# Performance work log

Measured on AMD Instinct MI355X. Metric: run time of the kernel, lower is better.

## Reference

```python
import jax, jax.numpy as jnp
import numpy as np

NUM_EXPERTS = 64
TOP_K = 2
B, S, EMB, MLP = 4, 2048, 1024, 2048


def setup_inputs() -> dict:
    key = jax.random.key(0)
    k1, k2, k3, k4, k5 = jax.random.split(key, 5)
    inputs = jax.random.normal(k1, (B, S, EMB), dtype=jnp.float32)
    gate_kernel = jax.random.normal(k2, (EMB, NUM_EXPERTS), dtype=jnp.float32) / np.sqrt(EMB)
    w0 = jax.random.normal(k3, (NUM_EXPERTS, EMB, MLP), dtype=jnp.float32) / np.sqrt(EMB)
    w1 = jax.random.normal(k4, (NUM_EXPERTS, EMB, MLP), dtype=jnp.float32) / np.sqrt(EMB)
    wo = jax.random.normal(k5, (NUM_EXPERTS, MLP, EMB), dtype=jnp.float32) / np.sqrt(MLP)
    return {"inputs": inputs, "gate_kernel": gate_kernel, "w0": w0, "w1": w1, "wo": wo}


def reference(inputs, gate_kernel, w0, w1, wo):
    b, s, e = inputs.shape
    x = inputs.reshape(b * s, e)                                  # [T, E]
    # Router (DenseGeneral gate)
    gate_logits = jnp.einsum('te,ex->tx', x, gate_kernel)         # [T, X]
    # permute(): top-k gating + sort tokens by expert
    weights, selected = jax.lax.top_k(gate_logits, TOP_K)         # [T, K]
    weights = jax.nn.softmax(weights.astype(jnp.float32), axis=-1)
    flat_experts = selected.reshape(-1)                           # [T*K]
    sort_idx = jnp.argsort(flat_experts)                          # [T*K]
    token_idx = sort_idx // TOP_K
    sorted_x = jnp.take(x, token_idx, axis=0)                     # [T*K, E]
    group_sizes = jnp.bincount(flat_experts, length=NUM_EXPERTS).astype(jnp.int32)
    # grouped GEMMs (gated FFN: silu(x@w0) * (x@w1) @ wo)
    h0 = jax.lax.ragged_dot(sorted_x, w0, group_sizes)            # [T*K, M]
    h1 = jax.lax.ragged_dot(sorted_x, w1, group_sizes)            # [T*K, M]
    inter = jax.nn.silu(h0) * h1
    out_sorted = jax.lax.ragged_dot(inter, wo, group_sizes)       # [T*K, E]
    # unpermute(): restore token order, weighted combine over top-k
    unsorted = jnp.take(out_sorted, jnp.argsort(sort_idx), axis=0)
    per_tok = unsorted.reshape(b * s, TOP_K, e)
    out = jnp.einsum('BKE,BK->BE', per_tok.astype(jnp.float32), weights)
    return out.reshape(b, s, e)
```

## Files before the change

kernel.cpp:

```cpp
#include <hip/hip_runtime.h>
#include <hip/hip_bf16.h>
#include <math.h>

#define NTOK   8192
#define NEXP   64
#define EMBD   1024
#define MLPD   2048
#define TOPK   2
#define NFLAT  (NTOK * TOPK)
#define BKD    32
#define MAXCH  8

typedef __attribute__((ext_vector_type(4)))  float  f32x4;
typedef __attribute__((ext_vector_type(16))) float  f32x16;
typedef __attribute__((ext_vector_type(8)))  __bf16 bf16x8;

__device__ __forceinline__ void gl16(const void* g, void* lds_base) {
  __builtin_amdgcn_global_load_lds(
      (const __attribute__((address_space(1))) unsigned int*)g,
      (__attribute__((address_space(3))) unsigned int*)lds_base, 16, 0, 0);
}
__device__ __forceinline__ void lgkm0_bar() {
  asm volatile("s_waitcnt lgkmcnt(0)" ::: "memory");
  __builtin_amdgcn_sched_barrier(0);
  __builtin_amdgcn_s_barrier();
}

#define OFF_COUNTS 0
#define OFF_BASE   256
#define OFF_RUN    512
#define OFF_EFLAT  1024
#define OFF_WFLAT  (1024 + 65536)
#define OFF_ROWTOK (1024 + 2 * 65536)
#define OFF_F2R    (1024 + 3 * 65536)
#define OFF_INTER  (1024 + 4 * 65536)
#define OFF_OS     (OFF_INTER + (size_t)NFLAT * MLPD * 2)
#define NEED_F32   (OFF_OS + (size_t)NFLAT * EMBD * 4)

__global__ __launch_bounds__(256) void router_topk(
    const float* __restrict__ x, const float* __restrict__ gk,
    int* __restrict__ e_flat, float* __restrict__ w_flat) {
  int t = blockIdx.x * 4 + (threadIdx.x >> 6);
  int l = threadIdx.x & 63;
  const float* xr = x + (size_t)t * EMBD;
  float acc = 0.f;
  #pragma unroll 8
  for (int i = 0; i < EMBD; ++i)
    acc = fmaf(xr[i], gk[i * NEXP + l], acc);
  float m = acc;
  for (int o = 32; o; o >>= 1) m = fmaxf(m, __shfl_xor(m, o));
  unsigned long long b1 = __ballot(acc == m);
  int i1 = __ffsll(b1) - 1;
  float v2 = (l == i1) ? -INFINITY : acc;
  float m2 = v2;
  for (int o = 32; o; o >>= 1) m2 = fmaxf(m2, __shfl_xor(m2, o));
  unsigned long long b2 = __ballot(v2 == m2);
  int i2 = __ffsll(b2) - 1;
  if (l == 0) {
    float e2 = expf(m2 - m);
    float inv = 1.f / (1.f + e2);
    e_flat[2 * t] = i1;  e_flat[2 * t + 1] = i2;
    w_flat[2 * t] = inv; w_flat[2 * t + 1] = e2 * inv;
  }
}

__global__ void hist_k(const int* __restrict__ ef, int* __restrict__ counts) {
  int j = blockIdx.x * 256 + threadIdx.x;
  if (j < NFLAT) atomicAdd(&counts[ef[j]], 1);
}

__global__ void scan_k(const int* __restrict__ counts, int* __restrict__ base) {
  if (threadIdx.x == 0) {
    int s = 0;
    for (int e = 0; e < NEXP; ++e) { base[e] = s; s += counts[e]; }
  }
}

__global__ void scatter_k(const int* __restrict__ ef, const int* __restrict__ base,
                          int* __restrict__ run, int* __restrict__ rowtok,
                          int* __restrict__ f2r) {
  int j = blockIdx.x * 256 + threadIdx.x;
  if (j < NFLAT) {
    int e = ef[j];
    int r = base[e] + atomicAdd(&run[e], 1);
    f2r[j] = r;
    rowtok[r] = j >> 1;
  }
}

__global__ __launch_bounds__(256, 3) void gemm1_k(
    const float* __restrict__ x, const float* __restrict__ w0,
    const float* __restrict__ w1, const int* __restrict__ counts,
    const int* __restrict__ base, const int* __restrict__ rowtok,
    __hip_bfloat16* __restrict__ inter) {
  int e = blockIdx.z;
  int Me = counts[e];
  int mc = blockIdx.y;
  if (mc * 128 >= Me) return;
  int rs = base[e];
  int nb = blockIdx.x * 64;
  int t = threadIdx.x;
  int wv = t >> 6, l = t & 63;
  int wr = wv >> 1, wc = wv & 1;
  int lo = l & 31, hi = l >> 5;

  __shared__ float Ash[4096];
  __shared__ float Bsh[2][4096];

  const float* abase0 = x;
  const float* abase1 = x;
  const float* wbase  = w0;
  if (wv < 2) {
    int g0 = wv * 2, g1 = wv * 2 + 1;
    int r0 = mc * 128 + g0 * 32 + lo; r0 = r0 < Me ? r0 : Me - 1;
    int r1 = mc * 128 + g1 * 32 + lo; r1 = r1 < Me ? r1 : Me - 1;
    abase0 = x + (size_t)rowtok[rs + r0] * EMBD + hi * 4;
    abase1 = x + (size_t)rowtok[rs + r1] * EMBD + hi * 4;
  } else {
    const float* w = (wv == 3) ? w1 : w0;
    wbase = w + (size_t)e * EMBD * MLPD + nb + (l & 15) * 4 + (size_t)(l >> 4) * MLPD;
  }
  int matofs = (wv & 1) * 2048;

  auto STAGE_A = [&](int kk) {
    #pragma unroll
    for (int h = 0; h < 4; ++h) {
      gl16(abase0 + kk + h * 8, &Ash[((wv * 2 + 0) * 4 + h) * 256]);
      gl16(abase1 + kk + h * 8, &Ash[((wv * 2 + 1) * 4 + h) * 256]);
    }
  };
  auto STAGE_B = [&](int buf, int kk) {
    #pragma unroll
    for (int j = 0; j < 8; ++j)
      gl16(wbase + (size_t)(kk + j * 4) * MLPD, &Bsh[buf][matofs + j * 256]);
  };

  f32x16 acc0[2], acc1[2];
  #pragma unroll
  for (int g = 0; g < 2; ++g)
    #pragma unroll
    for (int r = 0; r < 16; ++r) { acc0[g][r] = 0.f; acc1[g][r] = 0.f; }

  if (wv < 2) STAGE_A(0);
  else { STAGE_B(0, 0); STAGE_B(1, BKD); }

  const int NT = EMBD / BKD;
  for (int ks = 0; ks < NT; ++ks) {
    if (wv >= 2 && ks + 1 < NT) asm volatile("s_waitcnt vmcnt(8)" ::: "memory");
    else                        asm volatile("s_waitcnt vmcnt(0)" ::: "memory");
    __builtin_amdgcn_s_barrier();

    f32x4 a[2][2][2];
    #pragma unroll
    for (int g = 0; g < 2; ++g)
      #pragma unroll
      for (int kh = 0; kh < 2; ++kh) {
        int idx = (((wr * 2 + g) * 4 + kh * 2 + hi) * 256) + lo * 4;
        a[g][kh][0] = *(const f32x4*)&Ash[idx];
        a[g][kh][1] = *(const f32x4*)&Ash[idx + 128];
      }
    float b[2][2][8];
    const float* bb = Bsh[ks & 1];
    #pragma unroll
    for (int m = 0; m < 2; ++m)
      #pragma unroll
      for (int kh = 0; kh < 2; ++kh) {
        int bi = m * 2048 + (kh * 16 + hi * 8) * 64 + wc * 32 + lo;
        #pragma unroll
        for (int q = 0; q < 8; ++q) b[m][kh][q] = bb[bi + q * 64];
      }
    lgkm0_bar();
    if (wv < 2) { if (ks + 1 < NT) STAGE_A((ks + 1) * BKD); }
    else if (ks + 2 < NT) STAGE_B(ks & 1, (ks + 2) * BKD);

    bf16x8 av[2][2], bv[2][2];
    #pragma unroll
    for (int g = 0; g < 2; ++g)
      #pragma unroll
      for (int kh = 0; kh < 2; ++kh)
        #pragma unroll
        for (int q = 0; q < 4; ++q) {
          av[g][kh][q]     = (__bf16)a[g][kh][0][q];
          av[g][kh][4 + q] = (__bf16)a[g][kh][1][q];
        }
    #pragma unroll
    for (int m = 0; m < 2; ++m)
      #pragma unroll
      for (int kh = 0; kh < 2; ++kh)
        #pragma unroll
        for (int q = 0; q < 8; ++q) bv[m][kh][q] = (__bf16)b[m][kh][q];
    #pragma unroll
    for (int kh = 0; kh < 2; ++kh)
      #pragma unroll
      for (int g = 0; g < 2; ++g) {
        acc0[g] = __builtin_amdgcn_mfma_f32_32x32x16_bf16(av[g][kh], bv[0][kh], acc0[g], 0, 0, 0);
        acc1[g] = __builtin_amdgcn_mfma_f32_32x32x16_bf16(av[g][kh], bv[1][kh], acc1[g], 0, 0, 0);
      }
  }

  #pragma unroll
  for (int g = 0; g < 2; ++g)
    #pragma unroll
    for (int r = 0; r < 16; ++r) {
      int rl = mc * 128 + wr * 64 + g * 32 + (r & 3) + 8 * (r >> 2) + 4 * hi;
      if (rl < Me) {
        float h0 = acc0[g][r], h1 = acc1[g][r];
        float s = h0 / (1.f + expf(-h0)) * h1;
        inter[(size_t)(rs + rl) * MLPD + nb + wc * 32 + lo] = (__hip_bfloat16)s;
      }
    }
}

template <typename OS_T>
__global__ __launch_bounds__(256, 4) void gemm2_k(
    const __hip_bfloat16* __restrict__ inter, const float* __restrict__ wo,
    const int* __restrict__ counts, const int* __restrict__ base,
    OS_T* __restrict__ os) {
  int e = blockIdx.z;
  int Me = counts[e];
  int mc = blockIdx.y;
  if (mc * 128 >= Me) return;
  int rs = base[e];
  int nb = blockIdx.x * 64;
  int t = threadIdx.x;
  int wv = t >> 6, l = t & 63;
  int wr = wv >> 1, wc = wv & 1;
  int lo = l & 31, hi = l >> 5;

  __shared__ __bf16 A2[2][4096];
  __shared__ float  B2[2][2048];

  const __hip_bfloat16* ab0 = inter;
  const __hip_bfloat16* ab1 = inter;
  const float* wbase = wo;
  if (wv < 2) {
    int g0 = wv * 2, g1 = wv * 2 + 1;
    int r0 = mc * 128 + g0 * 32 + lo; r0 = r0 < Me ? r0 : Me - 1;
    int r1 = mc * 128 + g1 * 32 + lo; r1 = r1 < Me ? r1 : Me - 1;
    ab0 = inter + (size_t)(rs + r0) * MLPD + hi * 8;
    ab1 = inter + (size_t)(rs + r1) * MLPD + hi * 8;
  } else {
    wbase = wo + (size_t)e * MLPD * EMBD + nb + (l & 15) * 4 + (size_t)(l >> 4) * EMBD;
  }
  int jofs = (wv & 1) * 4;

  auto STAGE = [&](int buf, int kk) {
    if (wv < 2) {
      #pragma unroll
      for (int kh = 0; kh < 2; ++kh) {
        gl16(ab0 + kk + kh * 16, &A2[buf][((wv * 2 + 0) * 2 + kh) * 512]);
        gl16(ab1 + kk + kh * 16, &A2[buf][((wv * 2 + 1) * 2 + kh) * 512]);
      }
    } else {
      #pragma unroll
      for (int j = 0; j < 4; ++j)
        gl16(wbase + (size_t)(kk + (jofs + j) * 4) * EMBD, &B2[buf][(jofs + j) * 256]);
    }
  };

  f32x16 acc[2];
  #pragma unroll
  for (int g = 0; g < 2; ++g)
    #pragma unroll
    for (int r = 0; r < 16; ++r) acc[g][r] = 0.f;

  STAGE(0, 0);
  STAGE(1, BKD);
  const int NT = MLPD / BKD;
  for (int ks = 0; ks < NT; ++ks) {
    if (ks + 1 < NT) asm volatile("s_waitcnt vmcnt(4)" ::: "memory");
    else             asm volatile("s_waitcnt vmcnt(0)" ::: "memory");
    __builtin_amdgcn_s_barrier();

    bf16x8 av[2][2];
    #pragma unroll
    for (int g = 0; g < 2; ++g)
      #pragma unroll
      for (int kh = 0; kh < 2; ++kh)
        av[g][kh] = *(const bf16x8*)&A2[ks & 1][(((wr * 2 + g) * 2 + kh) * 512) + l * 8];
    float b[2][8];
    #pragma unroll
    for (int kh = 0; kh < 2; ++kh) {
      int bi = (kh * 16 + hi * 8) * 64 + wc * 32 + lo;
      #pragma unroll
      for (int q = 0; q < 8; ++q) b[kh][q] = B2[ks & 1][bi + q * 64];
    }
    lgkm0_bar();
    if (ks + 2 < NT) STAGE(ks & 1, (ks + 2) * BKD);

    bf16x8 bv[2];
    #pragma unroll
    for (int kh = 0; kh < 2; ++kh)
      #pragma unroll
      for (int q = 0; q < 8; ++q) bv[kh][q] = (__bf16)b[kh][q];
    #pragma unroll
    for (int kh = 0; kh < 2; ++kh)
      #pragma unroll
      for (int g = 0; g < 2; ++g)
        acc[g] = __builtin_amdgcn_mfma_f32_32x32x16_bf16(av[g][kh], bv[kh], acc[g], 0, 0, 0);
  }

  #pragma unroll
  for (int g = 0; g < 2; ++g)
    #pragma unroll
    for (int r = 0; r < 16; ++r) {
      int rl = mc * 128 + wr * 64 + g * 32 + (r & 3) + 8 * (r >> 2) + 4 * hi;
      if (rl < Me)
        os[(size_t)(rs + rl) * EMBD + nb + wc * 32 + lo] = (OS_T)acc[g][r];
    }
}

template <typename OS_T>
__global__ __launch_bounds__(256) void combine_k(
    const OS_T* __restrict__ os, const int* __restrict__ f2r,
    const float* __restrict__ wf, float* __restrict__ out) {
  int t = blockIdx.x;
  int c = threadIdx.x * 4;
  int r0 = f2r[2 * t], r1 = f2r[2 * t + 1];
  float wa = wf[2 * t], wb = wf[2 * t + 1];
  const OS_T* pa = os + (size_t)r0 * EMBD + c;
  const OS_T* pb = os + (size_t)r1 * EMBD + c;
  float4 o;
  o.x = wa * (float)pa[0] + wb * (float)pb[0];
  o.y = wa * (float)pa[1] + wb * (float)pb[1];
  o.z = wa * (float)pa[2] + wb * (float)pb[2];
  o.w = wa * (float)pa[3] + wb * (float)pb[3];
  *(float4*)(out + (size_t)t * EMBD + c) = o;
}

extern "C" void kernel_launch(void* const* d_in, const int* in_sizes, int n_in,
                              void* d_out, int out_size, void* d_ws, size_t ws_size,
                              hipStream_t stream) {
  const float* x  = (const float*)d_in[0];
  const float* gk = (const float*)d_in[1];
  const float* w0 = (const float*)d_in[2];
  const float* w1 = (const float*)d_in[3];
  const float* wo = (const float*)d_in[4];
  float* out = (float*)d_out;
  char* ws = (char*)d_ws;

  int*   counts = (int*)(ws + OFF_COUNTS);
  int*   basep  = (int*)(ws + OFF_BASE);
  int*   run    = (int*)(ws + OFF_RUN);
  int*   ef     = (int*)(ws + OFF_EFLAT);
  float* wfl    = (float*)(ws + OFF_WFLAT);
  int*   rowtok = (int*)(ws + OFF_ROWTOK);
  int*   f2r    = (int*)(ws + OFF_F2R);
  __hip_bfloat16* inter = (__hip_bfloat16*)(ws + OFF_INTER);

  hipMemsetAsync(ws, 0, 1024, stream);
  router_topk<<<NTOK / 4, 256, 0, stream>>>(x, gk, ef, wfl);
  hist_k<<<NFLAT / 256, 256, 0, stream>>>(ef, counts);
  scan_k<<<1, 64, 0, stream>>>(counts, basep);
  scatter_k<<<NFLAT / 256, 256, 0, stream>>>(ef, basep, run, rowtok, f2r);
  gemm1_k<<<dim3(MLPD / 64, MAXCH, NEXP), 256, 0, stream>>>(x, w0, w1, counts, basep, rowtok, inter);

  if (ws_size >= NEED_F32) {
    float* os = (float*)(ws + OFF_OS);
    gemm2_k<float><<<dim3(EMBD / 64, MAXCH, NEXP), 256, 0, stream>>>(inter, wo, counts, basep, os);
    combine_k<float><<<NTOK, 256, 0, stream>>>(os, f2r, wfl, out);
  } else {
    __hip_bfloat16* os = (__hip_bfloat16*)(ws + OFF_OS);
    gemm2_k<__hip_bfloat16><<<dim3(EMBD / 64, MAXCH, NEXP), 256, 0, stream>>>(inter, wo, counts, basep, os);
    combine_k<__hip_bfloat16><<<NTOK, 256, 0, stream>>>(os, f2r, wfl, out);
  }
}
```

Measured before the change: 1.087 ms.

## Load weight tiles straight into registers and double-buffer activations in LDS

Both grouped GEMM kernels change how they stage data. The weight (B) operand now goes straight from global memory into registers, prefetched two K-steps ahead, instead of being staged through LDS by dedicated waves. All four waves now share loading the activation (A) tile into a double-buffered LDS array. This removes the LDS round trip and the second barrier per step for B, at the cost of more registers (hence the lower occupancy hints in launch bounds) and duplicate B loads across the two row-waves.

```diff
diff --git a/kernel.cpp b/kernel.cpp
--- a/kernel.cpp
+++ b/kernel.cpp
@@ -19,11 +19,6 @@
   __builtin_amdgcn_global_load_lds(
       (const __attribute__((address_space(1))) unsigned int*)g,
       (__attribute__((address_space(3))) unsigned int*)lds_base, 16, 0, 0);
-}
-__device__ __forceinline__ void lgkm0_bar() {
-  asm volatile("s_waitcnt lgkmcnt(0)" ::: "memory");
-  __builtin_amdgcn_sched_barrier(0);
-  __builtin_amdgcn_s_barrier();
 }
 
 #define OFF_COUNTS 0
@@ -88,7 +83,7 @@
   }
 }
 
-__global__ __launch_bounds__(256, 3) void gemm1_k(
+__global__ __launch_bounds__(256, 2) void gemm1_k(
     const float* __restrict__ x, const float* __restrict__ w0,
     const float* __restrict__ w1, const int* __restrict__ counts,
     const int* __restrict__ base, const int* __restrict__ rowtok,
@@ -103,100 +98,88 @@
   int wv = t >> 6, l = t & 63;
   int wr = wv >> 1, wc = wv & 1;
   int lo = l & 31, hi = l >> 5;
-
-  __shared__ float Ash[4096];
-  __shared__ float Bsh[2][4096];
-
-  const float* abase0 = x;
-  const float* abase1 = x;
-  const float* wbase  = w0;
-  if (wv < 2) {
-    int g0 = wv * 2, g1 = wv * 2 + 1;
-    int r0 = mc * 128 + g0 * 32 + lo; r0 = r0 < Me ? r0 : Me - 1;
-    int r1 = mc * 128 + g1 * 32 + lo; r1 = r1 < Me ? r1 : Me - 1;
-    abase0 = x + (size_t)rowtok[rs + r0] * EMBD + hi * 4;
-    abase1 = x + (size_t)rowtok[rs + r1] * EMBD + hi * 4;
-  } else {
-    const float* w = (wv == 3) ? w1 : w0;
-    wbase = w + (size_t)e * EMBD * MLPD + nb + (l & 15) * 4 + (size_t)(l >> 4) * MLPD;
-  }
-  int matofs = (wv & 1) * 2048;
-
-  auto STAGE_A = [&](int kk) {
-    #pragma unroll
-    for (int h = 0; h < 4; ++h) {
-      gl16(abase0 + kk + h * 8, &Ash[((wv * 2 + 0) * 4 + h) * 256]);
-      gl16(abase1 + kk + h * 8, &Ash[((wv * 2 + 1) * 4 + h) * 256]);
-    }
-  };
-  auto STAGE_B = [&](int buf, int kk) {
-    #pragma unroll
-    for (int j = 0; j < 8; ++j)
-      gl16(wbase + (size_t)(kk + j * 4) * MLPD, &Bsh[buf][matofs + j * 256]);
-  };
-
+  int hi8 = hi * 8;
+
+  __shared__ float Ash[2][4096];
+
+  int rga = mc * 128 + wv * 32 + lo; rga = rga < Me ? rga : Me - 1;
+  const float* abase = x + (size_t)rowtok[rs + rga] * EMBD + hi * 4;
+  const float* bsrc0 = w0 + (size_t)e * EMBD * MLPD + nb + wc * 32 + lo;
+  const float* bsrc1 = w1 + (size_t)e * EMBD * MLPD + nb + wc * 32 + lo;
+
+  float br[2][2][2][8];
   f32x16 acc0[2], acc1[2];
   #pragma unroll
   for (int g = 0; g < 2; ++g)
     #pragma unroll
     for (int r = 0; r < 16; ++r) { acc0[g][r] = 0.f; acc1[g][r] = 0.f; }
 
-  if (wv < 2) STAGE_A(0);
-  else { STAGE_B(0, 0); STAGE_B(1, BKD); }
-
   const int NT = EMBD / BKD;
-  for (int ks = 0; ks < NT; ++ks) {
-    if (wv >= 2 && ks + 1 < NT) asm volatile("s_waitcnt vmcnt(8)" ::: "memory");
-    else                        asm volatile("s_waitcnt vmcnt(0)" ::: "memory");
-    __builtin_amdgcn_s_barrier();
-
-    f32x4 a[2][2][2];
-    #pragma unroll
-    for (int g = 0; g < 2; ++g)
-      #pragma unroll
-      for (int kh = 0; kh < 2; ++kh) {
-        int idx = (((wr * 2 + g) * 4 + kh * 2 + hi) * 256) + lo * 4;
-        a[g][kh][0] = *(const f32x4*)&Ash[idx];
-        a[g][kh][1] = *(const f32x4*)&Ash[idx + 128];
-      }
-    float b[2][2][8];
-    const float* bb = Bsh[ks & 1];
-    #pragma unroll
-    for (int m = 0; m < 2; ++m)
-      #pragma unroll
-      for (int kh = 0; kh < 2; ++kh) {
-        int bi = m * 2048 + (kh * 16 + hi * 8) * 64 + wc * 32 + lo;
-        #pragma unroll
-        for (int q = 0; q < 8; ++q) b[m][kh][q] = bb[bi + q * 64];
-      }
-    lgkm0_bar();
-    if (wv < 2) { if (ks + 1 < NT) STAGE_A((ks + 1) * BKD); }
-    else if (ks + 2 < NT) STAGE_B(ks & 1, (ks + 2) * BKD);
-
-    bf16x8 av[2][2], bv[2][2];
-    #pragma unroll
-    for (int g = 0; g < 2; ++g)
-      #pragma unroll
-      for (int kh = 0; kh < 2; ++kh)
-        #pragma unroll
-        for (int q = 0; q < 4; ++q) {
-          av[g][kh][q]     = (__bf16)a[g][kh][0][q];
-          av[g][kh][4 + q] = (__bf16)a[g][kh][1][q];
-        }
-    #pragma unroll
-    for (int m = 0; m < 2; ++m)
-      #pragma unroll
-      for (int kh = 0; kh < 2; ++kh)
-        #pragma unroll
-        for (int q = 0; q < 8; ++q) bv[m][kh][q] = (__bf16)b[m][kh][q];
+
+  #pragma unroll
+  for (int h = 0; h < 4; ++h)
+    gl16(abase + h * 8, &Ash[0][(wv * 4 + h) * 256]);
+  #pragma unroll
+  for (int m = 0; m < 2; ++m)
     #pragma unroll
     for (int kh = 0; kh < 2; ++kh)
       #pragma unroll
-      for (int g = 0; g < 2; ++g) {
-        acc0[g] = __builtin_amdgcn_mfma_f32_32x32x16_bf16(av[g][kh], bv[0][kh], acc0[g], 0, 0, 0);
-        acc1[g] = __builtin_amdgcn_mfma_f32_32x32x16_bf16(av[g][kh], bv[1][kh], acc1[g], 0, 0, 0);
+      for (int q = 0; q < 8; ++q) {
+        br[0][m][kh][q] = (m ? bsrc1 : bsrc0)[(size_t)(kh * 16 + hi8 + q) * MLPD];
+        br[1][m][kh][q] = (m ? bsrc1 : bsrc0)[(size_t)(BKD + kh * 16 + hi8 + q) * MLPD];
       }
-  }
+
+#define G1_PHASE(cur, ks)                                                           \
+  {                                                                                 \
+    if ((ks) + 1 < NT) asm volatile("s_waitcnt vmcnt(32)" ::: "memory");            \
+    else               asm volatile("s_waitcnt vmcnt(0)" ::: "memory");             \
+    __builtin_amdgcn_s_barrier();                                                   \
+    bf16x8 bv0[2], bv1[2];                                                          \
+    _Pragma("unroll")                                                               \
+    for (int kh = 0; kh < 2; ++kh)                                                  \
+      _Pragma("unroll")                                                             \
+      for (int q = 0; q < 8; ++q) {                                                 \
+        bv0[kh][q] = (__bf16)br[cur][0][kh][q];                                     \
+        bv1[kh][q] = (__bf16)br[cur][1][kh][q];                                     \
+      }                                                                             \
+    __builtin_amdgcn_sched_barrier(0);                                              \
+    if ((ks) + 1 < NT) {                                                            \
+      _Pragma("unroll")                                                             \
+      for (int h = 0; h < 4; ++h)                                                   \
+        gl16(abase + ((ks) + 1) * BKD + h * 8, &Ash[(cur) ^ 1][(wv * 4 + h) * 256]);\
+    }                                                                               \
+    __builtin_amdgcn_sched_barrier(0);                                              \
+    if ((ks) + 2 < NT) {                                                            \
+      _Pragma("unroll")                                                             \
+      for (int m = 0; m < 2; ++m)                                                   \
+        _Pragma("unroll")                                                           \
+        for (int kh = 0; kh < 2; ++kh)                                              \
+          _Pragma("unroll")                                                         \
+          for (int q = 0; q < 8; ++q)                                               \
+            br[cur][m][kh][q] = (m ? bsrc1 : bsrc0)[                                \
+                (size_t)(((ks) + 2) * BKD + kh * 16 + hi8 + q) * MLPD];             \
+    }                                                                               \
+    __builtin_amdgcn_sched_barrier(0);                                              \
+    _Pragma("unroll")                                                               \
+    for (int g = 0; g < 2; ++g)                                                     \
+      _Pragma("unroll")                                                             \
+      for (int kh = 0; kh < 2; ++kh) {                                              \
+        int idx = ((wr * 2 + g) * 4 + kh * 2 + hi) * 256 + lo * 4;                  \
+        f32x4 q0 = *(const f32x4*)&Ash[cur][idx];                                   \
+        f32x4 q1 = *(const f32x4*)&Ash[cur][idx + 128];                             \
+        bf16x8 av;                                                                  \
+        _Pragma("unroll")                                                           \
+        for (int q = 0; q < 4; ++q) { av[q] = (__bf16)q0[q]; av[4 + q] = (__bf16)q1[q]; } \
+        acc0[g] = __builtin_amdgcn_mfma_f32_32x32x16_bf16(av, bv0[kh], acc0[g], 0, 0, 0); \
+        acc1[g] = __builtin_amdgcn_mfma_f32_32x32x16_bf16(av, bv1[kh], acc1[g], 0, 0, 0); \
+      }                                                                             \
+  }
+
+  for (int ks = 0; ks < NT; ks += 2) {
+    G1_PHASE(0, ks);
+    G1_PHASE(1, ks + 1);
+  }
+#undef G1_PHASE
 
   #pragma unroll
   for (int g = 0; g < 2; ++g)
@@ -212,7 +195,7 @@
 }
 
 template <typename OS_T>
-__global__ __launch_bounds__(256, 4) void gemm2_k(
+__global__ __launch_bounds__(256, 3) void gemm2_k(
     const __hip_bfloat16* __restrict__ inter, const float* __restrict__ wo,
     const int* __restrict__ counts, const int* __restrict__ base,
     OS_T* __restrict__ os) {
@@ -226,79 +209,73 @@
   int wv = t >> 6, l = t & 63;
   int wr = wv >> 1, wc = wv & 1;
   int lo = l & 31, hi = l >> 5;
+  int hi8 = hi * 8;
 
   __shared__ __bf16 A2[2][4096];
-  __shared__ float  B2[2][2048];
-
-  const __hip_bfloat16* ab0 = inter;
-  const __hip_bfloat16* ab1 = inter;
-  const float* wbase = wo;
-  if (wv < 2) {
-    int g0 = wv * 2, g1 = wv * 2 + 1;
-    int r0 = mc * 128 + g0 * 32 + lo; r0 = r0 < Me ? r0 : Me - 1;
-    int r1 = mc * 128 + g1 * 32 + lo; r1 = r1 < Me ? r1 : Me - 1;
-    ab0 = inter + (size_t)(rs + r0) * MLPD + hi * 8;
-    ab1 = inter + (size_t)(rs + r1) * MLPD + hi * 8;
-  } else {
-    wbase = wo + (size_t)e * MLPD * EMBD + nb + (l & 15) * 4 + (size_t)(l >> 4) * EMBD;
-  }
-  int jofs = (wv & 1) * 4;
-
-  auto STAGE = [&](int buf, int kk) {
-    if (wv < 2) {
-      #pragma unroll
-      for (int kh = 0; kh < 2; ++kh) {
-        gl16(ab0 + kk + kh * 16, &A2[buf][((wv * 2 + 0) * 2 + kh) * 512]);
-        gl16(ab1 + kk + kh * 16, &A2[buf][((wv * 2 + 1) * 2 + kh) * 512]);
-      }
-    } else {
-      #pragma unroll
-      for (int j = 0; j < 4; ++j)
-        gl16(wbase + (size_t)(kk + (jofs + j) * 4) * EMBD, &B2[buf][(jofs + j) * 256]);
+
+  int rga = mc * 128 + wv * 32 + lo; rga = rga < Me ? rga : Me - 1;
+  const __hip_bfloat16* ab = inter + (size_t)(rs + rga) * MLPD + hi8;
+  const float* bsrc = wo + (size_t)e * MLPD * EMBD + nb + wc * 32 + lo;
+
+  float br[2][2][8];
+  f32x16 acc[2];
+  #pragma unroll
+  for (int g = 0; g < 2; ++g)
+    #pragma unroll
+    for (int r = 0; r < 16; ++r) acc[g][r] = 0.f;
+
+  const int NT = MLPD / BKD;
+
+  #pragma unroll
+  for (int kh = 0; kh < 2; ++kh)
+    gl16(ab + kh * 16, &A2[0][(wv * 2 + kh) * 512]);
+  #pragma unroll
+  for (int kh = 0; kh < 2; ++kh)
+    #pragma unroll
+    for (int q = 0; q < 8; ++q) {
+      br[0][kh][q] = bsrc[(size_t)(kh * 16 + hi8 + q) * EMBD];
+      br[1][kh][q] = bsrc[(size_t)(BKD + kh * 16 + hi8 + q) * EMBD];
     }
-  };
-
-  f32x16 acc[2];
-  #pragma unroll
-  for (int g = 0; g < 2; ++g)
-    #pragma unroll
-    for (int r = 0; r < 16; ++r) acc[g][r] = 0.f;
-
-  STAGE(0, 0);
-  STAGE(1, BKD);
-  const int NT = MLPD / BKD;
-  for (int ks = 0; ks < NT; ++ks) {
-    if (ks + 1 < NT) asm volatile("s_waitcnt vmcnt(4)" ::: "memory");
-    else             asm volatile("s_waitcnt vmcnt(0)" ::: "memory");
-    __builtin_amdgcn_s_barrier();
-
-    bf16x8 av[2][2];
-    #pragma unroll
-    for (int g = 0; g < 2; ++g)
-      #pragma unroll
-      for (int kh = 0; kh < 2; ++kh)
-        av[g][kh] = *(const bf16x8*)&A2[ks & 1][(((wr * 2 + g) * 2 + kh) * 512) + l * 8];
-    float b[2][8];
-    #pragma unroll
-    for (int kh = 0; kh < 2; ++kh) {
-      int bi = (kh * 16 + hi * 8) * 64 + wc * 32 + lo;
-      #pragma unroll
-      for (int q = 0; q < 8; ++q) b[kh][q] = B2[ks & 1][bi + q * 64];
-    }
-    lgkm0_bar();
-    if (ks + 2 < NT) STAGE(ks & 1, (ks + 2) * BKD);
-
-    bf16x8 bv[2];
-    #pragma unroll
-    for (int kh = 0; kh < 2; ++kh)
-      #pragma unroll
-      for (int q = 0; q < 8; ++q) bv[kh][q] = (__bf16)b[kh][q];
-    #pragma unroll
-    for (int kh = 0; kh < 2; ++kh)
-      #pragma unroll
-      for (int g = 0; g < 2; ++g)
-        acc[g] = __builtin_amdgcn_mfma_f32_32x32x16_bf16(av[g][kh], bv[kh], acc[g], 0, 0, 0);
-  }
+
+#define G2_PHASE(cur, ks)                                                           \
+  {                                                                                 \
+    if ((ks) + 1 < NT) asm volatile("s_waitcnt vmcnt(16)" ::: "memory");            \
+    else               asm volatile("s_waitcnt vmcnt(0)" ::: "memory");             \
+    __builtin_amdgcn_s_barrier();                                                   \
+    bf16x8 bv[2];                                                                   \
+    _Pragma("unroll")                                                               \
+    for (int kh = 0; kh < 2; ++kh)                                                  \
+      _Pragma("unroll")                                                             \
+      for (int q = 0; q < 8; ++q) bv[kh][q] = (__bf16)br[cur][kh][q];               \
+    __builtin_amdgcn_sched_barrier(0);                                              \
+    if ((ks) + 1 < NT) {                                                            \
+      _Pragma("unroll")                                                             \
+      for (int kh = 0; kh < 2; ++kh)                                                \
+        gl16(ab + ((ks) + 1) * BKD + kh * 16, &A2[(cur) ^ 1][(wv * 2 + kh) * 512]); \
+    }                                                                               \
+    __builtin_amdgcn_sched_barrier(0);                                              \
+    if ((ks) + 2 < NT) {                                                            \
+      _Pragma("unroll")                                                             \
+      for (int kh = 0; kh < 2; ++kh)                                                \
+        _Pragma("unroll")                                                           \
+        for (int q = 0; q < 8; ++q)                                                 \
+          br[cur][kh][q] = bsrc[(size_t)(((ks) + 2) * BKD + kh * 16 + hi8 + q) * EMBD]; \
+    }                                                                               \
+    __builtin_amdgcn_sched_barrier(0);                                              \
+    _Pragma("unroll")                                                               \
+    for (int g = 0; g < 2; ++g)                                                     \
+      _Pragma("unroll")                                                             \
+      for (int kh = 0; kh < 2; ++kh) {                                              \
+        bf16x8 av = *(const bf16x8*)&A2[cur][((wr * 2 + g) * 2 + kh) * 512 + l * 8];\
+        acc[g] = __builtin_amdgcn_mfma_f32_32x32x16_bf16(av, bv[kh], acc[g], 0, 0, 0); \
+      }                                                                             \
+  }
+
+  for (int ks = 0; ks < NT; ks += 2) {
+    G2_PHASE(0, ks);
+    G2_PHASE(1, ks + 1);
+  }
+#undef G2_PHASE
 
   #pragma unroll
   for (int g = 0; g < 2; ++g)
```

Result: slower. 1.140 ms (+4.9%).

## Pre-convert activations to bf16 and triple-buffer both grouped GEMM pipelines

Applied to the files above, without the earlier changes.

A new kernel converts the input activations to bf16 once, so gemm1 gathers half as many bytes per row and no longer converts A in its inner loop. Both GEMMs move from double to triple-buffered LDS staging, with all four waves sharing the A and B loads. The next-next tile is issued right after the barrier, which removes the second LDS-drain barrier per iteration. The cost is an extra conversion pass over x, more LDS per block, and lower occupancy hints. The bf16 buffer reuses the output scratch region, which is safe only because gemm1 finishes before gemm2 writes there.

```diff
diff --git a/kernel.cpp b/kernel.cpp
--- a/kernel.cpp
+++ b/kernel.cpp
@@ -19,11 +19,6 @@
   __builtin_amdgcn_global_load_lds(
       (const __attribute__((address_space(1))) unsigned int*)g,
       (__attribute__((address_space(3))) unsigned int*)lds_base, 16, 0, 0);
-}
-__device__ __forceinline__ void lgkm0_bar() {
-  asm volatile("s_waitcnt lgkmcnt(0)" ::: "memory");
-  __builtin_amdgcn_sched_barrier(0);
-  __builtin_amdgcn_s_barrier();
 }
 
 #define OFF_COUNTS 0
@@ -35,7 +30,19 @@
 #define OFF_F2R    (1024 + 3 * 65536)
 #define OFF_INTER  (1024 + 4 * 65536)
 #define OFF_OS     (OFF_INTER + (size_t)NFLAT * MLPD * 2)
+#define OFF_XB     OFF_OS
 #define NEED_F32   (OFF_OS + (size_t)NFLAT * EMBD * 4)
+
+__global__ __launch_bounds__(256) void cvt_x_k(const float* __restrict__ x,
+                                               __bf16* __restrict__ xb) {
+  size_t i = ((size_t)blockIdx.x * 256 + threadIdx.x) * 8;
+  f32x4 f0 = *(const f32x4*)(x + i);
+  f32x4 f1 = *(const f32x4*)(x + i + 4);
+  bf16x8 v;
+  #pragma unroll
+  for (int q = 0; q < 4; ++q) { v[q] = (__bf16)f0[q]; v[4 + q] = (__bf16)f1[q]; }
+  *(bf16x8*)(xb + i) = v;
+}
 
 __global__ __launch_bounds__(256) void router_topk(
     const float* __restrict__ x, const float* __restrict__ gk,
@@ -88,8 +95,8 @@
   }
 }
 
-__global__ __launch_bounds__(256, 3) void gemm1_k(
-    const float* __restrict__ x, const float* __restrict__ w0,
+__global__ __launch_bounds__(256, 2) void gemm1_k(
+    const __bf16* __restrict__ xb, const float* __restrict__ w0,
     const float* __restrict__ w1, const int* __restrict__ counts,
     const int* __restrict__ base, const int* __restrict__ rowtok,
     __hip_bfloat16* __restrict__ inter) {
@@ -104,36 +111,26 @@
   int wr = wv >> 1, wc = wv & 1;
   int lo = l & 31, hi = l >> 5;
 
-  __shared__ float Ash[4096];
-  __shared__ float Bsh[2][4096];
-
-  const float* abase0 = x;
-  const float* abase1 = x;
-  const float* wbase  = w0;
-  if (wv < 2) {
-    int g0 = wv * 2, g1 = wv * 2 + 1;
-    int r0 = mc * 128 + g0 * 32 + lo; r0 = r0 < Me ? r0 : Me - 1;
-    int r1 = mc * 128 + g1 * 32 + lo; r1 = r1 < Me ? r1 : Me - 1;
-    abase0 = x + (size_t)rowtok[rs + r0] * EMBD + hi * 4;
-    abase1 = x + (size_t)rowtok[rs + r1] * EMBD + hi * 4;
-  } else {
-    const float* w = (wv == 3) ? w1 : w0;
-    wbase = w + (size_t)e * EMBD * MLPD + nb + (l & 15) * 4 + (size_t)(l >> 4) * MLPD;
-  }
-  int matofs = (wv & 1) * 2048;
-
-  auto STAGE_A = [&](int kk) {
-    #pragma unroll
-    for (int h = 0; h < 4; ++h) {
-      gl16(abase0 + kk + h * 8, &Ash[((wv * 2 + 0) * 4 + h) * 256]);
-      gl16(abase1 + kk + h * 8, &Ash[((wv * 2 + 1) * 4 + h) * 256]);
-    }
+  __shared__ __bf16 A1[3][4096];
+  __shared__ float  B1[3][4096];
+
+  int rga = mc * 128 + wv * 32 + lo; rga = rga < Me ? rga : Me - 1;
+  const __bf16* abase = xb + (size_t)rowtok[rs + rga] * EMBD + hi * 8;
+  int bm = wv >> 1, bk0 = (wv & 1) * 16;
+  const float* wsel = bm ? w1 : w0;
+  const float* wbase = wsel + (size_t)e * EMBD * MLPD + nb + (l & 15) * 4 +
+                       (size_t)(l >> 4) * MLPD;
+
+  auto STAGE = [&](int ks, int buf) {
+    int kk = ks * BKD;
+    #pragma unroll
+    for (int kh = 0; kh < 2; ++kh)
+      gl16(abase + kk + kh * 16, &A1[buf][(wv * 2 + kh) * 512]);
+    #pragma unroll
+    for (int j = 0; j < 4; ++j)
+      gl16(wbase + (size_t)(kk + bk0 + j * 4) * MLPD,
+           &B1[buf][bm * 2048 + (bk0 + j * 4) * 64]);
   };
-  auto STAGE_B = [&](int buf, int kk) {
-    #pragma unroll
-    for (int j = 0; j < 8; ++j)
-      gl16(wbase + (size_t)(kk + j * 4) * MLPD, &Bsh[buf][matofs + j * 256]);
-  };
 
   f32x16 acc0[2], acc1[2];
   #pragma unroll
@@ -141,61 +138,49 @@
     #pragma unroll
     for (int r = 0; r < 16; ++r) { acc0[g][r] = 0.f; acc1[g][r] = 0.f; }
 
-  if (wv < 2) STAGE_A(0);
-  else { STAGE_B(0, 0); STAGE_B(1, BKD); }
-
   const int NT = EMBD / BKD;
+  STAGE(0, 0);
+  STAGE(1, 1);
+  int bufR = 0, bufW = 2;
   for (int ks = 0; ks < NT; ++ks) {
-    if (wv >= 2 && ks + 1 < NT) asm volatile("s_waitcnt vmcnt(8)" ::: "memory");
-    else                        asm volatile("s_waitcnt vmcnt(0)" ::: "memory");
+    if (ks + 1 < NT) asm volatile("s_waitcnt vmcnt(6)" ::: "memory");
+    else             asm volatile("s_waitcnt vmcnt(0)" ::: "memory");
+    __builtin_amdgcn_sched_barrier(0);
     __builtin_amdgcn_s_barrier();
-
-    f32x4 a[2][2][2];
+    if (ks + 2 < NT) STAGE(ks + 2, bufW);
+
+    bf16x8 av[2][2];
     #pragma unroll
     for (int g = 0; g < 2; ++g)
       #pragma unroll
-      for (int kh = 0; kh < 2; ++kh) {
-        int idx = (((wr * 2 + g) * 4 + kh * 2 + hi) * 256) + lo * 4;
-        a[g][kh][0] = *(const f32x4*)&Ash[idx];
-        a[g][kh][1] = *(const f32x4*)&Ash[idx + 128];
-      }
+      for (int kh = 0; kh < 2; ++kh)
+        av[g][kh] = *(const bf16x8*)&A1[bufR][((wr * 2 + g) * 2 + kh) * 512 + l * 8];
     float b[2][2][8];
-    const float* bb = Bsh[ks & 1];
     #pragma unroll
     for (int m = 0; m < 2; ++m)
       #pragma unroll
       for (int kh = 0; kh < 2; ++kh) {
         int bi = m * 2048 + (kh * 16 + hi * 8) * 64 + wc * 32 + lo;
         #pragma unroll
-        for (int q = 0; q < 8; ++q) b[m][kh][q] = bb[bi + q * 64];
+        for (int q = 0; q < 8; ++q) b[m][kh][q] = B1[bufR][bi + q * 64];
       }
-    lgkm0_bar();
-    if (wv < 2) { if (ks + 1 < NT) STAGE_A((ks + 1) * BKD); }
-    else if (ks + 2 < NT) STAGE_B(ks & 1, (ks + 2) * BKD);
-
-    bf16x8 av[2][2], bv[2][2];
-    #pragma unroll
-    for (int g = 0; g < 2; ++g)
-      #pragma unroll
-      for (int kh = 0; kh < 2; ++kh)
-        #pragma unroll
-        for (int q = 0; q < 4; ++q) {
-          av[g][kh][q]     = (__bf16)a[g][kh][0][q];
-          av[g][kh][4 + q] = (__bf16)a[g][kh][1][q];
-        }
-    #pragma unroll
-    for (int m = 0; m < 2; ++m)
-      #pragma unroll
-      for (int kh = 0; kh < 2; ++kh)
-        #pragma unroll
-        for (int q = 0; q < 8; ++q) bv[m][kh][q] = (__bf16)b[m][kh][q];
+    bf16x8 bv0[2], bv1[2];
+    #pragma unroll
+    for (int kh = 0; kh < 2; ++kh)
+      #pragma unroll
+      for (int q = 0; q < 8; ++q) {
+        bv0[kh][q] = (__bf16)b[0][kh][q];
+        bv1[kh][q] = (__bf16)b[1][kh][q];
+      }
     #pragma unroll
     for (int kh = 0; kh < 2; ++kh)
       #pragma unroll
       for (int g = 0; g < 2; ++g) {
-        acc0[g] = __builtin_amdgcn_mfma_f32_32x32x16_bf16(av[g][kh], bv[0][kh], acc0[g], 0, 0, 0);
-        acc1[g] = __builtin_amdgcn_mfma_f32_32x32x16_bf16(av[g][kh], bv[1][kh], acc1[g], 0, 0, 0);
+        acc0[g] = __builtin_amdgcn_mfma_f32_32x32x16_bf16(av[g][kh], bv0[kh], acc0[g], 0, 0, 0);
+        acc1[g] = __builtin_amdgcn_mfma_f32_32x32x16_bf16(av[g][kh], bv1[kh], acc1[g], 0, 0, 0);
       }
+    bufR = bufR == 2 ? 0 : bufR + 1;
+    bufW = bufW == 2 ? 0 : bufW + 1;
   }
 
   #pragma unroll
@@ -212,7 +197,7 @@
 }
 
 template <typename OS_T>
-__global__ __launch_bounds__(256, 4) void gemm2_k(
+__global__ __launch_bounds__(256, 3) void gemm2_k(
     const __hip_bfloat16* __restrict__ inter, const float* __restrict__ wo,
     const int* __restrict__ counts, const int* __restrict__ base,
     OS_T* __restrict__ os) {
@@ -227,35 +212,23 @@
   int wr = wv >> 1, wc = wv & 1;
   int lo = l & 31, hi = l >> 5;
 
-  __shared__ __bf16 A2[2][4096];
-  __shared__ float  B2[2][2048];
-
-  const __hip_bfloat16* ab0 = inter;
-  const __hip_bfloat16* ab1 = inter;
-  const float* wbase = wo;
-  if (wv < 2) {
-    int g0 = wv * 2, g1 = wv * 2 + 1;
-    int r0 = mc * 128 + g0 * 32 + lo; r0 = r0 < Me ? r0 : Me - 1;
-    int r1 = mc * 128 + g1 * 32 + lo; r1 = r1 < Me ? r1 : Me - 1;
-    ab0 = inter + (size_t)(rs + r0) * MLPD + hi * 8;
-    ab1 = inter + (size_t)(rs + r1) * MLPD + hi * 8;
-  } else {
-    wbase = wo + (size_t)e * MLPD * EMBD + nb + (l & 15) * 4 + (size_t)(l >> 4) * EMBD;
-  }
-  int jofs = (wv & 1) * 4;
-
-  auto STAGE = [&](int buf, int kk) {
-    if (wv < 2) {
-      #pragma unroll
-      for (int kh = 0; kh < 2; ++kh) {
-        gl16(ab0 + kk + kh * 16, &A2[buf][((wv * 2 + 0) * 2 + kh) * 512]);
-        gl16(ab1 + kk + kh * 16, &A2[buf][((wv * 2 + 1) * 2 + kh) * 512]);
-      }
-    } else {
-      #pragma unroll
-      for (int j = 0; j < 4; ++j)
-        gl16(wbase + (size_t)(kk + (jofs + j) * 4) * EMBD, &B2[buf][(jofs + j) * 256]);
-    }
+  __shared__ __bf16 A2[3][4096];
+  __shared__ float  B2[3][2048];
+
+  int rga = mc * 128 + wv * 32 + lo; rga = rga < Me ? rga : Me - 1;
+  const __bf16* abase = (const __bf16*)inter + (size_t)(rs + rga) * MLPD + hi * 8;
+  const float* wbase = wo + (size_t)e * MLPD * EMBD + nb + (l & 15) * 4 +
+                       (size_t)(l >> 4) * EMBD;
+
+  auto STAGE = [&](int ks, int buf) {
+    int kk = ks * BKD;
+    #pragma unroll
+    for (int kh = 0; kh < 2; ++kh)
+      gl16(abase + kk + kh * 16, &A2[buf][(wv * 2 + kh) * 512]);
+    #pragma unroll
+    for (int j = 0; j < 2; ++j)
+      gl16(wbase + (size_t)(kk + wv * 8 + j * 4) * EMBD,
+           &B2[buf][(wv * 8 + j * 4) * 64]);
   };
 
   f32x16 acc[2];
@@ -264,30 +237,30 @@
     #pragma unroll
     for (int r = 0; r < 16; ++r) acc[g][r] = 0.f;
 
+  const int NT = MLPD / BKD;
   STAGE(0, 0);
-  STAGE(1, BKD);
-  const int NT = MLPD / BKD;
+  STAGE(1, 1);
+  int bufR = 0, bufW = 2;
   for (int ks = 0; ks < NT; ++ks) {
     if (ks + 1 < NT) asm volatile("s_waitcnt vmcnt(4)" ::: "memory");
     else             asm volatile("s_waitcnt vmcnt(0)" ::: "memory");
+    __builtin_amdgcn_sched_barrier(0);
     __builtin_amdgcn_s_barrier();
+    if (ks + 2 < NT) STAGE(ks + 2, bufW);
 
     bf16x8 av[2][2];
     #pragma unroll
     for (int g = 0; g < 2; ++g)
       #pragma unroll
       for (int kh = 0; kh < 2; ++kh)
-        av[g][kh] = *(const bf16x8*)&A2[ks & 1][(((wr * 2 + g) * 2 + kh) * 512) + l * 8];
+        av[g][kh] = *(const bf16x8*)&A2[bufR][((wr * 2 + g) * 2 + kh) * 512 + l * 8];
     float b[2][8];
     #pragma unroll
     for (int kh = 0; kh < 2; ++kh) {
       int bi = (kh * 16 + hi * 8) * 64 + wc * 32 + lo;
       #pragma unroll
-      for (int q = 0; q < 8; ++q) b[kh][q] = B2[ks & 1][bi + q * 64];
+      for (int q = 0; q < 8; ++q) b[kh][q] = B2[bufR][bi + q * 64];
     }
-    lgkm0_bar();
-    if (ks + 2 < NT) STAGE(ks & 1, (ks + 2) * BKD);
-
     bf16x8 bv[2];
     #pragma unroll
     for (int kh = 0; kh < 2; ++kh)
@@ -298,6 +271,8 @@
       #pragma unroll
       for (int g = 0; g < 2; ++g)
         acc[g] = __builtin_amdgcn_mfma_f32_32x32x16_bf16(av[g][kh], bv[kh], acc[g], 0, 0, 0);
+    bufR = bufR == 2 ? 0 : bufR + 1;
+    bufW = bufW == 2 ? 0 : bufW + 1;
   }
 
   #pragma unroll
@@ -347,13 +322,15 @@
   int*   rowtok = (int*)(ws + OFF_ROWTOK);
   int*   f2r    = (int*)(ws + OFF_F2R);
   __hip_bfloat16* inter = (__hip_bfloat16*)(ws + OFF_INTER);
+  __bf16* xb = (__bf16*)(ws + OFF_XB);
 
   hipMemsetAsync(ws, 0, 1024, stream);
+  cvt_x_k<<<NTOK * EMBD / (256 * 8), 256, 0, stream>>>(x, xb);
   router_topk<<<NTOK / 4, 256, 0, stream>>>(x, gk, ef, wfl);
   hist_k<<<NFLAT / 256, 256, 0, stream>>>(ef, counts);
   scan_k<<<1, 64, 0, stream>>>(counts, basep);
   scatter_k<<<NFLAT / 256, 256, 0, stream>>>(ef, basep, run, rowtok, f2r);
-  gemm1_k<<<dim3(MLPD / 64, MAXCH, NEXP), 256, 0, stream>>>(x, w0, w1, counts, basep, rowtok, inter);
+  gemm1_k<<<dim3(MLPD / 64, MAXCH, NEXP), 256, 0, stream>>>(xb, w0, w1, counts, basep, rowtok, inter);
 
   if (ws_size >= NEED_F32) {
     float* os = (float*)(ws + OFF_OS);
```

After: 938.0 us. 1.16x faster.
